# Kernel tuning notes

Hardware: AMD Instinct MI355X
Metric: run time of the kernel (lower is better)

Reference implementation:

```python
import jax, jax.numpy as jnp
import numpy as np

L = 16            # number_of_grid_levels
T = 524288        # max_hash_table_entries (2^19)
F = 2             # hash_table_feature_dim
MIN_RES = 16      # coarsest_resolution
MAX_RES = 2048    # finest_resolution
WIDTH = 64        # mlp_width
OUT = 3           # output_channels
N = 1048576       # number of 2D query points
PRIME_Y = np.uint32(2654435761)  # NGP spatial hash prime for dim 1 (dim 0 prime = 1)


def _resolutions():
    g = np.exp((np.log(MAX_RES) - np.log(MIN_RES)) / (L - 1))
    return np.floor(MIN_RES * g ** np.arange(L)).astype(np.float32)  # [L]


def setup_inputs() -> dict:
    key = jax.random.key(0)
    ks = jax.random.split(key, 6)
    x = jax.random.uniform(ks[0], (N, 2), dtype=jnp.float32)
    # NGP hash tables are initialized small uniform
    tables = jax.random.uniform(ks[1], (L, T, F), minval=-1e-4, maxval=1e-4, dtype=jnp.float32)
    def dense(k, fi, fo):
        return (jax.random.normal(k, (fi, fo), dtype=jnp.float32) / np.sqrt(fi).astype(np.float32))
    W0 = dense(ks[2], L * F, WIDTH)
    W1 = dense(ks[3], WIDTH, WIDTH)
    W2 = dense(ks[4], WIDTH, OUT)
    return dict(x=x, tables=tables,
                W0=W0, b0=jnp.zeros((WIDTH,), jnp.float32),
                W1=W1, b1=jnp.zeros((WIDTH,), jnp.float32),
                W2=W2, b2=jnp.zeros((OUT,), jnp.float32))


def _hash_encode(x, tables):
    # Multi-resolution hash grid encoding (Instant-NGP, spatial_dim=2).
    res = jnp.asarray(_resolutions())                  # [L]
    scaled = x[:, None, :] * res[None, :, None]        # [N, L, 2]
    floored = jnp.floor(scaled)
    frac = scaled - floored                            # [N, L, 2]
    corners = jnp.array([[0, 0], [1, 0], [0, 1], [1, 1]], dtype=jnp.int32)  # [4, 2]
    vert = floored.astype(jnp.int32)[:, :, None, :] + corners[None, None]   # [N, L, 4, 2]
    vu = vert.astype(jnp.uint32)
    h = vu[..., 0] ^ (vu[..., 1] * PRIME_Y)            # spatial hash (prime for dim0 is 1)
    idx = (h % jnp.uint32(T)).astype(jnp.int32)        # [N, L, 4]
    feats = tables[jnp.arange(L)[None, :, None], idx]  # [N, L, 4, F] gather per level
    # bilinear weights: prod over dims of frac (if corner==1) else 1-frac
    wd = jnp.where(corners[None, None] == 1, frac[:, :, None, :], 1.0 - frac[:, :, None, :])
    w = wd[..., 0] * wd[..., 1]                        # [N, L, 4]
    interp = jnp.einsum('nlc,nlcf->nlf', w, feats)     # [N, L, F]
    return interp.reshape(x.shape[0], L * F)           # [N, L*F]


def reference(x, tables, W0, b0, W1, b1, W2, b2):
    h = _hash_encode(x, tables)
    h = jax.nn.relu(h @ W0 + b0)
    h = jax.nn.relu(h @ W1 + b1)
    return jax.nn.sigmoid(h @ W2 + b2)   # [N, 3]
```

## Files before the change

### kernel.cpp

```cpp
#include <hip/hip_runtime.h>

#define LVLS  16
#define TSZ   524288u
#define TMASK (TSZ - 1u)
#define PRIME 2654435761u

__constant__ float RES[LVLS] = {16.f, 22.f, 30.f, 42.f, 58.f, 80.f, 111.f, 153.f,
                                212.f, 294.f, 406.f, 561.f, 776.f, 1072.f, 1482.f, 2048.f};

typedef __bf16 bf16x8 __attribute__((ext_vector_type(8)));
typedef float  f32x4  __attribute__((ext_vector_type(4)));

union Frag {
    uint4          q;
    unsigned       u[4];
    unsigned short s[8];
    bf16x8         v;
};

static __device__ __forceinline__ unsigned short f2bf(float f) {
    unsigned u = __float_as_uint(f);
    u += 0x7FFFu + ((u >> 16) & 1u);
    return (unsigned short)(u >> 16);
}
static __device__ __forceinline__ unsigned pack2(float a, float b) {
    return (unsigned)f2bf(a) | ((unsigned)f2bf(b) << 16);
}
static __device__ __forceinline__ void lds_fence() {
    asm volatile("s_waitcnt lgkmcnt(0)" ::: "memory");
}

static __device__ __forceinline__ unsigned encode_level(
    const float2 xy, const float res, const float* __restrict__ tbf)
{
    const float sx = xy.x * res, sy = xy.y * res;
    const float fx = floorf(sx),  fy = floorf(sy);
    const float ux = sx - fx,     uy = sy - fy;
    const unsigned ix = (unsigned)(int)fx, iy = (unsigned)(int)fy;
    const unsigned hy0 = iy * PRIME, hy1 = (iy + 1u) * PRIME;
    const unsigned i00 = (ix ^ hy0) & TMASK;
    const unsigned i01 = (ix ^ hy1) & TMASK;
    float2 f00, f10, f01, f11;
    if (!(ix & 1u)) {
        const f32x4 a = *(const f32x4*)(tbf + 2u * (i00 & ~1u));
        const f32x4 b = *(const f32x4*)(tbf + 2u * (i01 & ~1u));
        const bool s0 = (i00 & 1u) != 0u;
        const bool s1 = (i01 & 1u) != 0u;
        f00 = s0 ? make_float2(a[2], a[3]) : make_float2(a[0], a[1]);
        f10 = s0 ? make_float2(a[0], a[1]) : make_float2(a[2], a[3]);
        f01 = s1 ? make_float2(b[2], b[3]) : make_float2(b[0], b[1]);
        f11 = s1 ? make_float2(b[0], b[1]) : make_float2(b[2], b[3]);
    } else {
        const unsigned i10 = ((ix + 1u) ^ hy0) & TMASK;
        const unsigned i11 = ((ix + 1u) ^ hy1) & TMASK;
        const float2* tb2 = (const float2*)tbf;
        f00 = tb2[i00]; f10 = tb2[i10];
        f01 = tb2[i01]; f11 = tb2[i11];
    }
    const float w00 = (1.f - ux) * (1.f - uy);
    const float w10 = ux * (1.f - uy);
    const float w01 = (1.f - ux) * uy;
    const float w11 = ux * uy;
    const float e0 = w00*f00.x + w10*f10.x + w01*f01.x + w11*f11.x;
    const float e1 = w00*f00.y + w10*f10.y + w01*f01.y + w11*f11.y;
    return pack2(e0, e1);
}

__global__ __launch_bounds__(256) void ngp_encode_fine(
    const float* __restrict__ x, const float* __restrict__ tables,
    unsigned* __restrict__ feat, int N)
{
    const int g = blockIdx.x;
    const int r = g & 7;
    const int l = 8 + r;
    const int n = (g >> 3) * 256 + (int)threadIdx.x;
    if (n >= N) return;
    const float2 xy = ((const float2*)x)[n];
    const float* tbf = tables + (size_t)l * (TSZ * 2u);
    feat[(size_t)r * N + n] = encode_level(xy, RES[l], tbf);
}

#define CLVL 8
#define SFEAT_BYTES (8 * CLVL * 64 * 4)
#define SB0_BYTES   (4 * 64 * 16)
#define HSCR_BYTES  (8 * 16 * 72 * 2)

__global__ __launch_bounds__(512, 4) void ngp_fused(
    const float* __restrict__ x, const float* __restrict__ tables,
    const unsigned* __restrict__ feat,
    const float* __restrict__ W0, const float* __restrict__ b0,
    const float* __restrict__ W1, const float* __restrict__ b1,
    const float* __restrict__ W2, const float* __restrict__ b2,
    float* __restrict__ out, int N)
{
    __shared__ __align__(16) unsigned char smem[SFEAT_BYTES + HSCR_BYTES];
    unsigned* sfeat = (unsigned*)smem;
    uint4*    sB0   = (uint4*)(smem + SFEAT_BYTES);
    uint4*    sB1   = (uint4*)(smem + SFEAT_BYTES + SB0_BYTES);
    unsigned short (*hscr)[16][72] =
        (unsigned short (*)[16][72])(smem + SFEAT_BYTES);

    const int tid  = threadIdx.x;
    const int lane = tid & 63;
    const int w    = tid >> 6;
    const int c    = lane & 15;
    const int quad = lane >> 4;

    {
        const int f = w;
        if (f < 4) {
            Frag t0;
            #pragma unroll
            for (int j = 0; j < 8; ++j)
                t0.s[j] = f2bf(W0[(quad * 8 + j) * 64 + f * 16 + c]);
            sB0[f * 64 + lane] = t0.q;
        }
        {
            const int kt = f >> 2, tt = f & 3;
            Frag t1;
            #pragma unroll
            for (int j = 0; j < 8; ++j)
                t1.s[j] = f2bf(W1[(kt * 32 + quad * 8 + j) * 64 + tt * 16 + c]);
            sB1[f * 64 + lane] = t1.q;
        }
    }

    const int n = blockIdx.x * 512 + tid;
    if (n < N) {
        const float2 xy = ((const float2*)x)[n];
        #pragma unroll 4
        for (int l = 0; l < CLVL; ++l) {
            const float* tbf = tables + (size_t)l * (TSZ * 2u);
            const unsigned p = encode_level(xy, RES[l], tbf);
            sfeat[(w * CLVL + l) * 64 + (lane ^ (((l >> 2) & 1) << 4))] = p;
        }
    }
    __syncthreads();

    Frag B0f[4], B1f[8], B2f[2];
    #pragma unroll
    for (int t = 0; t < 4; ++t) B0f[t].q = sB0[t * 64 + lane];
    #pragma unroll
    for (int f = 0; f < 8; ++f) B1f[f].q = sB1[f * 64 + lane];
    #pragma unroll
    for (int f = 0; f < 2; ++f) {
        #pragma unroll
        for (int j = 0; j < 8; ++j) {
            const float v = (c < 3) ? W2[(f * 32 + quad * 8 + j) * 3 + c] : 0.f;
            B2f[f].s[j] = f2bf(v);
        }
    }

    float bias0[4], bias1[4];
    #pragma unroll
    for (int t = 0; t < 4; ++t) { bias0[t] = b0[t * 16 + c]; bias1[t] = b1[t * 16 + c]; }
    const float bias2 = (c < 3) ? b2[c] : 0.f;

    __syncthreads();

    #pragma unroll 1
    for (int it = 0; it < 4; ++it) {
        const int n0 = blockIdx.x * 512 + w * 64 + it * 16;

        Frag a0;
        if (quad < 2) {
            #pragma unroll
            for (int i = 0; i < 4; ++i)
                a0.u[i] = sfeat[(w * CLVL + quad * 4 + i) * 64 + ((it * 16 + c) ^ (quad << 4))];
        } else {
            #pragma unroll
            for (int i = 0; i < 4; ++i)
                a0.u[i] = feat[(size_t)((quad - 2) * 4 + i) * N + n0 + c];
        }

        f32x4 acc0[4];
        #pragma unroll
        for (int t = 0; t < 4; ++t) {
            f32x4 cin = {bias0[t], bias0[t], bias0[t], bias0[t]};
            acc0[t] = __builtin_amdgcn_mfma_f32_16x16x32_bf16(a0.v, B0f[t].v, cin, 0, 0, 0);
        }

        lds_fence();
        #pragma unroll
        for (int t = 0; t < 4; ++t)
            #pragma unroll
            for (int rr = 0; rr < 4; ++rr)
                hscr[w][quad * 4 + rr][t * 16 + c] = f2bf(fmaxf(acc0[t][rr], 0.f));

        lds_fence();
        Frag a1[2];
        #pragma unroll
        for (int kt = 0; kt < 2; ++kt)
            a1[kt].q = *(const uint4*)&hscr[w][c][kt * 32 + quad * 8];

        f32x4 acc1[4];
        #pragma unroll
        for (int t = 0; t < 4; ++t) {
            f32x4 cin = {bias1[t], bias1[t], bias1[t], bias1[t]};
            cin = __builtin_amdgcn_mfma_f32_16x16x32_bf16(a1[0].v, B1f[t].v, cin, 0, 0, 0);
            acc1[t] = __builtin_amdgcn_mfma_f32_16x16x32_bf16(a1[1].v, B1f[4 + t].v, cin, 0, 0, 0);
        }

        lds_fence();
        #pragma unroll
        for (int t = 0; t < 4; ++t)
            #pragma unroll
            for (int rr = 0; rr < 4; ++rr)
                hscr[w][quad * 4 + rr][t * 16 + c] = f2bf(fmaxf(acc1[t][rr], 0.f));

        lds_fence();
        Frag a2[2];
        #pragma unroll
        for (int kt = 0; kt < 2; ++kt)
            a2[kt].q = *(const uint4*)&hscr[w][c][kt * 32 + quad * 8];

        f32x4 cin2 = {bias2, bias2, bias2, bias2};
        cin2 = __builtin_amdgcn_mfma_f32_16x16x32_bf16(a2[0].v, B2f[0].v, cin2, 0, 0, 0);
        f32x4 acc2 = __builtin_amdgcn_mfma_f32_16x16x32_bf16(a2[1].v, B2f[1].v, cin2, 0, 0, 0);

        if (c < 3) {
            #pragma unroll
            for (int rr = 0; rr < 4; ++rr) {
                if (n0 + quad * 4 + rr < N) {
                    const float s = 1.f / (1.f + __expf(-acc2[rr]));
                    out[(size_t)(n0 + quad * 4 + rr) * 3 + c] = s;
                }
            }
        }
    }
}

extern "C" void kernel_launch(void* const* d_in, const int* in_sizes, int n_in,
                              void* d_out, int out_size, void* d_ws, size_t ws_size,
                              hipStream_t stream) {
    const float* x      = (const float*)d_in[0];
    const float* tables = (const float*)d_in[1];
    const float* W0     = (const float*)d_in[2];
    const float* b0     = (const float*)d_in[3];
    const float* W1     = (const float*)d_in[4];
    const float* b1     = (const float*)d_in[5];
    const float* W2     = (const float*)d_in[6];
    const float* b2     = (const float*)d_in[7];
    float* out = (float*)d_out;
    unsigned* feat = (unsigned*)d_ws;
    (void)ws_size; (void)n_in; (void)out_size;

    const int N  = in_sizes[0] / 2;
    const int FB = (N + 255) / 256;
    const int PB = (N + 511) / 512;
    ngp_encode_fine<<<8 * FB, 256, 0, stream>>>(x, tables, feat, N);
    ngp_fused<<<PB, 512, 0, stream>>>(x, tables, feat, W0, b0, W1, b1, W2, b2, out, N);
}
```

Measured before the change: 267.9 us.

## Dehash coarse levels into dense grid staged in shared memory

Adds a small kernel that gathers the hash-table entries for the four coarsest levels (grid vertices up to 43x43) into a compact dense array in the workspace. The fused kernel copies this array into LDS and does bilinear interpolation for levels 0-3 from shared memory instead of issuing random global gathers. This removes scattered global loads for the coarse levels, at the cost of about 29 KB more LDS per block, which may lower occupancy, plus an extra barrier and a tiny extra launch.

After: 260.5 us. 1.03x faster.

```diff
diff --git a/kernel.cpp b/kernel.cpp
--- a/kernel.cpp
+++ b/kernel.cpp
@@ -66,6 +66,25 @@
     return pack2(e0, e1);
 }
 
+#define DENSE_TOTAL 3628
+
+__global__ __launch_bounds__(256) void ngp_dehash(
+    const float* __restrict__ tables, float2* __restrict__ dense)
+{
+    const int e = blockIdx.x * 256 + (int)threadIdx.x;
+    if (e >= DENSE_TOTAL) return;
+    int l, base;
+    if      (e >= 1779) { l = 3; base = 1779; }
+    else if (e >=  818) { l = 2; base =  818; }
+    else if (e >=  289) { l = 1; base =  289; }
+    else                { l = 0; base =    0; }
+    const int Wd = (l == 0) ? 17 : (l == 1) ? 23 : (l == 2) ? 31 : 43;
+    const int r  = e - base;
+    const unsigned iy = (unsigned)(r / Wd), ix = (unsigned)(r % Wd);
+    const unsigned h = (ix ^ (iy * PRIME)) & TMASK;
+    dense[e] = ((const float2*)(tables + (size_t)l * (TSZ * 2u)))[h];
+}
+
 __global__ __launch_bounds__(256) void ngp_encode_fine(
     const float* __restrict__ x, const float* __restrict__ tables,
     unsigned* __restrict__ feat, int N)
@@ -83,20 +102,24 @@
 #define CLVL 8
 #define SFEAT_BYTES (8 * CLVL * 64 * 4)
 #define SB0_BYTES   (4 * 64 * 16)
-#define HSCR_BYTES  (8 * 16 * 72 * 2)
+#define SB1_BYTES   (8 * 64 * 16)
+#define SDENSE_BYTES (DENSE_TOTAL * 8)
+#define REGION_BYTES (SB0_BYTES + SB1_BYTES + SDENSE_BYTES)
 
 __global__ __launch_bounds__(512, 4) void ngp_fused(
     const float* __restrict__ x, const float* __restrict__ tables,
+    const float2* __restrict__ dense_g,
     const unsigned* __restrict__ feat,
     const float* __restrict__ W0, const float* __restrict__ b0,
     const float* __restrict__ W1, const float* __restrict__ b1,
     const float* __restrict__ W2, const float* __restrict__ b2,
     float* __restrict__ out, int N)
 {
-    __shared__ __align__(16) unsigned char smem[SFEAT_BYTES + HSCR_BYTES];
+    __shared__ __align__(16) unsigned char smem[SFEAT_BYTES + REGION_BYTES];
     unsigned* sfeat = (unsigned*)smem;
     uint4*    sB0   = (uint4*)(smem + SFEAT_BYTES);
     uint4*    sB1   = (uint4*)(smem + SFEAT_BYTES + SB0_BYTES);
+    float2*   sdense = (float2*)(smem + SFEAT_BYTES + SB0_BYTES + SB1_BYTES);
     unsigned short (*hscr)[16][72] =
         (unsigned short (*)[16][72])(smem + SFEAT_BYTES);
 
@@ -123,13 +146,36 @@
                 t1.s[j] = f2bf(W1[(kt * 32 + quad * 8 + j) * 64 + tt * 16 + c]);
             sB1[f * 64 + lane] = t1.q;
         }
-    }
+        for (int e = tid; e < DENSE_TOTAL; e += 512)
+            sdense[e] = dense_g[e];
+    }
+    __syncthreads();
 
     const int n = blockIdx.x * 512 + tid;
     if (n < N) {
         const float2 xy = ((const float2*)x)[n];
-        #pragma unroll 4
-        for (int l = 0; l < CLVL; ++l) {
+        #pragma unroll
+        for (int l = 0; l < 4; ++l) {
+            const int off = (l == 0) ? 0 : (l == 1) ? 289 : (l == 2) ? 818 : 1779;
+            const int Wd  = (l == 0) ? 17 : (l == 1) ? 23 : (l == 2) ? 31 : 43;
+            const float res = RES[l];
+            const float sx = xy.x * res, sy = xy.y * res;
+            const float fx = floorf(sx),  fy = floorf(sy);
+            const float ux = sx - fx,     uy = sy - fy;
+            const int ix = (int)fx, iy = (int)fy;
+            const int b = off + iy * Wd + ix;
+            const float2 f00 = sdense[b],      f10 = sdense[b + 1];
+            const float2 f01 = sdense[b + Wd], f11 = sdense[b + Wd + 1];
+            const float w00 = (1.f - ux) * (1.f - uy);
+            const float w10 = ux * (1.f - uy);
+            const float w01 = (1.f - ux) * uy;
+            const float w11 = ux * uy;
+            const float e0 = w00*f00.x + w10*f10.x + w01*f01.x + w11*f11.x;
+            const float e1 = w00*f00.y + w10*f10.y + w01*f01.y + w11*f11.y;
+            sfeat[(w * CLVL + l) * 64 + (lane ^ (((l >> 2) & 1) << 4))] = pack2(e0, e1);
+        }
+        #pragma unroll 2
+        for (int l = 4; l < CLVL; ++l) {
             const float* tbf = tables + (size_t)l * (TSZ * 2u);
             const unsigned p = encode_level(xy, RES[l], tbf);
             sfeat[(w * CLVL + l) * 64 + (lane ^ (((l >> 2) & 1) << 4))] = p;
@@ -242,12 +288,16 @@
     const float* W2     = (const float*)d_in[6];
     const float* b2     = (const float*)d_in[7];
     float* out = (float*)d_out;
-    unsigned* feat = (unsigned*)d_ws;
     (void)ws_size; (void)n_in; (void)out_size;
 
     const int N  = in_sizes[0] / 2;
+    unsigned* feat  = (unsigned*)d_ws;
+    float2*   dense = (float2*)((char*)d_ws + (size_t)8 * N * 4);
+
     const int FB = (N + 255) / 256;
     const int PB = (N + 511) / 512;
+    ngp_dehash<<<(DENSE_TOTAL + 255) / 256, 256, 0, stream>>>(tables, dense);
     ngp_encode_fine<<<8 * FB, 256, 0, stream>>>(x, tables, feat, N);
-    ngp_fused<<<PB, 512, 0, stream>>>(x, tables, feat, W0, b0, W1, b1, W2, b2, out, N);
-}
+    ngp_fused<<<PB, 512, 0, stream>>>(x, tables, dense, feat,
+                                      W0, b0, W1, b1, W2, b2, out, N);
+}
```
